# Kernel optimization log

Hardware: AMD Instinct MI355X
Metric: run time of the kernel (lower is better)

## Reference

```python
import jax, jax.numpy as jnp
import numpy as np

IN_DIM = 1024
D_QK = IN_DIM // 8  # 128


def setup_inputs() -> dict:
    key = jax.random.key(0)
    ks = jax.random.split(key, 8)
    B, S, H = 8, 2048, IN_DIM
    x = jax.random.normal(ks[0], (B, S, H), dtype=jnp.float32)
    s = 1.0 / np.sqrt(H)
    Wq = jax.random.uniform(ks[1], (H, D_QK), jnp.float32, -s, s)
    bq = jax.random.uniform(ks[2], (D_QK,), jnp.float32, -s, s)
    Wk = jax.random.uniform(ks[3], (H, D_QK), jnp.float32, -s, s)
    bk = jax.random.uniform(ks[4], (D_QK,), jnp.float32, -s, s)
    Wv = jax.random.uniform(ks[5], (H, H), jnp.float32, -s, s)
    bv = jax.random.uniform(ks[6], (H,), jnp.float32, -s, s)
    # nn.Parameter(torch.zeros(1)) in the original; use a small random value so
    # the residual-gated branch is exercised.
    gamma = jax.random.normal(ks[7], (1,), dtype=jnp.float32) * 0.1
    return {"x": x, "Wq": Wq, "bq": bq, "Wk": Wk, "bk": bk,
            "Wv": Wv, "bv": bv, "gamma": gamma}


def reference(x, Wq, bq, Wk, bk, Wv, bv, gamma):
    # x: [B, S, H]
    q = jnp.einsum('bsh,hd->bsd', x, Wq) + bq          # [B, S, D_QK]
    k = jnp.einsum('bsh,hd->bsd', x, Wk) + bk          # [B, S, D_QK]
    v = jnp.einsum('bsh,hg->bsg', x, Wv) + bv          # [B, S, H]
    energy = jnp.einsum('bsd,btd->bst', q, k)          # [B, S, S] (no 1/sqrt(d) scale, as in original)
    attention = jax.nn.softmax(energy, axis=-1)
    out = jnp.einsum('bst,bth->bsh', attention, v)     # [B, S, H]
    return gamma * out + x
```

## Files before the change

### kernel.cpp

```cpp
#include <hip/hip_runtime.h>
#include <hip/hip_bf16.h>
#include <stdint.h>


typedef __attribute__((ext_vector_type(8))) short bf16x8;
typedef __attribute__((ext_vector_type(8))) unsigned short u16x8;
typedef __attribute__((ext_vector_type(4))) float f32x4;

#define S_LEN 2048
#define NB 8
#define HDIM 1024
#define MTOT (NB * S_LEN)
#define NQKV 1280

__device__ __forceinline__ unsigned short f2b(float f) {
  union { float f; unsigned u; } v; v.f = f;
  unsigned u = v.u;
  return (unsigned short)((u + 0x7FFFu + ((u >> 16) & 1u)) >> 16);
}
__device__ __forceinline__ float b2f(unsigned short h) {
  union { unsigned u; float f; } v; v.u = ((unsigned)h) << 16; return v.f;
}

__device__ __forceinline__ void gload16(const void* g, void* l) {
  __builtin_amdgcn_global_load_lds((const __attribute__((address_space(1))) void*)g,
                                   (__attribute__((address_space(3))) void*)l,
                                   16, 0, 0);
}

__global__ void k_cast_x(const float* __restrict__ x, unsigned short* __restrict__ xb) {
  int i = blockIdx.x * blockDim.x + threadIdx.x;
  const float4* xv = (const float4*)x;
  float4 a = xv[2 * i], b = xv[2 * i + 1];
  u16x8 o;
  o[0] = f2b(a.x); o[1] = f2b(a.y); o[2] = f2b(a.z); o[3] = f2b(a.w);
  o[4] = f2b(b.x); o[5] = f2b(b.y); o[6] = f2b(b.z); o[7] = f2b(b.w);
  *(u16x8*)(xb + 8 * (size_t)i) = o;
}

__global__ void k_build_w(const float* __restrict__ Wq, const float* __restrict__ bq,
                          const float* __restrict__ Wk, const float* __restrict__ bk,
                          const float* __restrict__ Wv, const float* __restrict__ bv,
                          unsigned short* __restrict__ wt, float* __restrict__ bc) {
  int i = blockIdx.x * 256 + threadIdx.x;
  int n = i >> 10, h = i & 1023;
  float v;
  if (n < 128)      v = Wq[h * 128 + n];
  else if (n < 256) v = Wk[h * 128 + n - 128];
  else              v = Wv[h * 1024 + n - 256];
  wt[i] = f2b(v);
  if (i < NQKV) bc[i] = (i < 128) ? bq[i] : (i < 256) ? bk[i - 128] : bv[i - 256];
}

__launch_bounds__(256, 2)
__global__ void k_gemm_qkv(const unsigned short* __restrict__ A,
                           const unsigned short* __restrict__ Bt,
                           const float* __restrict__ bc,
                           unsigned short* __restrict__ C) {
  __shared__ unsigned short smem[2 * 128 * 32];
  unsigned short* As = smem;
  unsigned short* Bs = smem + 128 * 32;
  const int tid = threadIdx.x;
  const int m0 = blockIdx.x * 128, n0 = blockIdx.y * 128;
  const int l = tid & 63, wid = tid >> 6;
  const int wm = wid >> 1, wn = wid & 1;
  const int l15 = l & 15, lh = l >> 4;
  const int r0 = tid >> 2, seg = tid & 3;
  f32x4 acc[4][4] = {};
  for (int kt = 0; kt < 32; ++kt) {
#pragma unroll
    for (int p = 0; p < 2; ++p) {
      int row = p * 64 + r0;
      gload16(A  + (size_t)(m0 + row) * 1024 + kt * 32 + seg * 8, As + (size_t)(p * 256 + tid) * 8);
      gload16(Bt + (size_t)(n0 + row) * 1024 + kt * 32 + seg * 8, Bs + (size_t)(p * 256 + tid) * 8);
    }
    __syncthreads();
    bf16x8 af[4], bfr[4];
#pragma unroll
    for (int mi = 0; mi < 4; ++mi)
      af[mi] = *(const bf16x8*)&As[(wm * 64 + mi * 16 + l15) * 32 + 8 * lh];
#pragma unroll
    for (int ni = 0; ni < 4; ++ni)
      bfr[ni] = *(const bf16x8*)&Bs[(wn * 64 + ni * 16 + l15) * 32 + 8 * lh];
#pragma unroll
    for (int mi = 0; mi < 4; ++mi)
#pragma unroll
      for (int ni = 0; ni < 4; ++ni)
        acc[mi][ni] = __builtin_amdgcn_mfma_f32_16x16x32_bf16(af[mi], bfr[ni], acc[mi][ni], 0, 0, 0);
    __syncthreads();
  }
  unsigned short* sc = As + wid * 1024;
  const int erow = l >> 2, ech = l & 3;
  for (int mi = 0; mi < 4; ++mi) {
    asm volatile("s_waitcnt lgkmcnt(0)" ::: "memory");
#pragma unroll
    for (int ni = 0; ni < 4; ++ni) {
      float bias = bc[n0 + wn * 64 + ni * 16 + l15];
#pragma unroll
      for (int r = 0; r < 4; ++r) {
        int row = lh * 4 + r;
        int col = (ni * 16 + l15) ^ ((row & 7) * 8);
        sc[row * 64 + col] = f2b(acc[mi][ni][r] + bias);
      }
    }
    asm volatile("s_waitcnt lgkmcnt(0)" ::: "memory");
    int gr = m0 + wm * 64 + mi * 16 + erow;
#pragma unroll
    for (int h = 0; h < 2; ++h) {
      int ch = ech + h * 4;
      int colsw = (ch ^ (erow & 7)) * 8;
      u16x8 vv = *(const u16x8*)(sc + erow * 64 + colsw);
      *(u16x8*)(&C[(size_t)gr * NQKV + n0 + wn * 64 + ch * 8]) = vv;
    }
  }
}

__launch_bounds__(512, 2)
__global__ void k_scores(const unsigned short* __restrict__ qkv, unsigned short* __restrict__ P) {
  __shared__ unsigned short E[16 * 2048];
  const int tid = threadIdx.x;
  const int l = tid & 63, w = tid >> 6;
  const int l15 = l & 15, lh = l >> 4;
  const int b = blockIdx.y, q0 = blockIdx.x * 16;
  const size_t base = (size_t)(b * S_LEN) * NQKV;

  bf16x8 qf[4];
  const unsigned short* qrow = qkv + base + (size_t)(q0 + l15) * NQKV + 8 * lh;
#pragma unroll
  for (int d0 = 0; d0 < 4; ++d0) qf[d0] = *(const bf16x8*)(qrow + d0 * 32);

  for (int i = 0; i < 16; ++i) {
    int k0 = (w * 16 + i) * 16;
    const unsigned short* krow = qkv + base + (size_t)(k0 + l15) * NQKV + 128 + 8 * lh;
    f32x4 e = {};
#pragma unroll
    for (int d0 = 0; d0 < 4; ++d0) {
      bf16x8 kf = *(const bf16x8*)(krow + d0 * 32);
      e = __builtin_amdgcn_mfma_f32_16x16x32_bf16(qf[d0], kf, e, 0, 0, 0);
    }
#pragma unroll
    for (int r = 0; r < 4; ++r) {
      int row = lh * 4 + r;
      E[row * 2048 + ((k0 + l15) ^ (row * 8))] = f2b(e[r]);
    }
  }
  __syncthreads();

  const int r = tid >> 5, g = tid & 31;
  unsigned short* Er = &E[r * 2048];
  float mx = -3e38f;
#pragma unroll
  for (int j = 0; j < 8; ++j) {
    u16x8 v = *(const u16x8*)(Er + g * 8 + j * 256);
#pragma unroll
    for (int t = 0; t < 8; ++t) mx = fmaxf(mx, b2f(v[t]));
  }
#pragma unroll
  for (int o = 16; o; o >>= 1) mx = fmaxf(mx, __shfl_xor(mx, o));
  float sum = 0.f;
#pragma unroll
  for (int j = 0; j < 8; ++j) {
    u16x8 v = *(const u16x8*)(Er + g * 8 + j * 256);
    u16x8 ov;
#pragma unroll
    for (int t = 0; t < 8; ++t) { float e = __expf(b2f(v[t]) - mx); sum += e; ov[t] = f2b(e); }
    *(u16x8*)(Er + g * 8 + j * 256) = ov;
  }
#pragma unroll
  for (int o = 16; o; o >>= 1) sum += __shfl_xor(sum, o);
  const float inv = 1.f / sum;
  unsigned short* Pr = P + ((size_t)(b * S_LEN + q0 + r)) * S_LEN;
#pragma unroll
  for (int j = 0; j < 8; ++j) {
    int idx = g * 8 + j * 256;
    u16x8 v = *(const u16x8*)(Er + idx);
    u16x8 ov;
#pragma unroll
    for (int t = 0; t < 8; ++t) ov[t] = f2b(b2f(v[t]) * inv);
    *(u16x8*)(Pr + (idx ^ (r * 8))) = ov;
  }
}

__global__ void k_transpose_v(const unsigned short* __restrict__ qkv, unsigned short* __restrict__ vt) {
  __shared__ unsigned short t[64][66];
  const int m0 = blockIdx.x * 64, c0 = blockIdx.y * 64;
  const int tx = threadIdx.x & 63, ty = threadIdx.x >> 6;
#pragma unroll
  for (int i = 0; i < 64; i += 4)
    t[ty + i][tx] = qkv[(size_t)(m0 + ty + i) * NQKV + 256 + c0 + tx];
  __syncthreads();
#pragma unroll
  for (int i = 0; i < 64; i += 4)
    vt[(size_t)(c0 + ty + i) * MTOT + m0 + tx] = t[tx][ty + i];
}

__launch_bounds__(256, 2)
__global__ void k_gemm_pv(const unsigned short* __restrict__ P,
                          const unsigned short* __restrict__ Vt,
                          const float* __restrict__ x,
                          const float* __restrict__ gamma,
                          float* __restrict__ out) {
  __shared__ unsigned short smem[2 * 128 * 32];
  unsigned short* As = smem;
  unsigned short* Bs = smem + 128 * 32;
  const int tid = threadIdx.x;
  const int b = blockIdx.z;
  const int m0 = blockIdx.x * 128, n0 = blockIdx.y * 128;
  const int l = tid & 63, wid = tid >> 6;
  const int wm = wid >> 1, wn = wid & 1;
  const int l15 = l & 15, lh = l >> 4;
  const int r0 = tid >> 2, seg = tid & 3;
  const unsigned short* Ab = P + (size_t)b * S_LEN * S_LEN;
  f32x4 acc[4][4] = {};
  for (int kt = 0; kt < 64; ++kt) {
#pragma unroll
    for (int p = 0; p < 2; ++p) {
      int row = p * 64 + r0;
      gload16(Ab + (size_t)(m0 + row) * S_LEN + kt * 32 + seg * 8, As + (size_t)(p * 256 + tid) * 8);
      gload16(Vt + (size_t)(n0 + row) * MTOT + b * S_LEN + kt * 32 + seg * 8, Bs + (size_t)(p * 256 + tid) * 8);
    }
    __syncthreads();
    bf16x8 af[4], bfr[4];
#pragma unroll
    for (int mi = 0; mi < 4; ++mi)
      af[mi] = *(const bf16x8*)&As[(wm * 64 + mi * 16 + l15) * 32 + 8 * lh];
#pragma unroll
    for (int ni = 0; ni < 4; ++ni)
      bfr[ni] = *(const bf16x8*)&Bs[(wn * 64 + ni * 16 + l15) * 32 + 8 * lh];
#pragma unroll
    for (int mi = 0; mi < 4; ++mi)
#pragma unroll
      for (int ni = 0; ni < 4; ++ni)
        acc[mi][ni] = __builtin_amdgcn_mfma_f32_16x16x32_bf16(af[mi], bfr[ni], acc[mi][ni], 0, 0, 0);
    __syncthreads();
  }
  const float gm = gamma[0];
  float* sc = (float*)smem + wid * 1024;
  const int erow = l >> 2, ech = l & 3;
  for (int mi = 0; mi < 4; ++mi) {
    asm volatile("s_waitcnt lgkmcnt(0)" ::: "memory");
#pragma unroll
    for (int ni = 0; ni < 4; ++ni)
#pragma unroll
      for (int r = 0; r < 4; ++r) {
        int row = lh * 4 + r;
        int col = (ni * 16 + l15) ^ (row * 4);
        sc[row * 64 + col] = acc[mi][ni][r];
      }
    asm volatile("s_waitcnt lgkmcnt(0)" ::: "memory");
    int gr = b * S_LEN + m0 + wm * 64 + mi * 16 + erow;
#pragma unroll
    for (int h = 0; h < 4; ++h) {
      int ch = ech + h * 4;
      int colsw = (ch ^ erow) * 4;
      f32x4 vv = *(const f32x4*)(sc + erow * 64 + colsw);
      size_t o = (size_t)gr * HDIM + n0 + wn * 64 + ch * 4;
      float4 xv = *(const float4*)(x + o);
      float4 ov;
      ov.x = gm * vv[0] + xv.x; ov.y = gm * vv[1] + xv.y;
      ov.z = gm * vv[2] + xv.z; ov.w = gm * vv[3] + xv.w;
      *(float4*)(out + o) = ov;
    }
  }
}

extern "C" void kernel_launch(void* const* d_in, const int* in_sizes, int n_in,
                              void* d_out, int out_size, void* d_ws, size_t ws_size,
                              hipStream_t stream) {
  const float* x     = (const float*)d_in[0];
  const float* Wq    = (const float*)d_in[1];
  const float* bq    = (const float*)d_in[2];
  const float* Wk    = (const float*)d_in[3];
  const float* bk    = (const float*)d_in[4];
  const float* Wv    = (const float*)d_in[5];
  const float* bv    = (const float*)d_in[6];
  const float* gamma = (const float*)d_in[7];
  float* out = (float*)d_out;
  char* ws = (char*)d_ws;

  unsigned short* xb  = (unsigned short*)(ws);
  unsigned short* wt  = (unsigned short*)(ws + 33554432);
  float*          bc  = (float*)         (ws + 36175872);
  unsigned short* qkv = (unsigned short*)(ws + 36180992);
  unsigned short* P   = (unsigned short*)(ws + 78124032);
  unsigned short* vt  = xb;

  hipLaunchKernelGGL(k_cast_x,      dim3(8192),      dim3(256), 0, stream, x, xb);
  hipLaunchKernelGGL(k_build_w,     dim3(5120),      dim3(256), 0, stream, Wq, bq, Wk, bk, Wv, bv, wt, bc);
  hipLaunchKernelGGL(k_gemm_qkv,    dim3(128, 10),   dim3(256), 0, stream, xb, wt, bc, qkv);
  hipLaunchKernelGGL(k_scores,      dim3(128, 8),    dim3(512), 0, stream, qkv, P);
  hipLaunchKernelGGL(k_transpose_v, dim3(256, 16),   dim3(256), 0, stream, qkv, vt);
  hipLaunchKernelGGL(k_gemm_pv,     dim3(16, 8, 8),  dim3(256), 0, stream, P, vt, x, gamma, out);
}
```

Measured before the change: 366.7 us.

## Fuse scores, softmax and PV GEMM into one two-pass attention kernel

Replaces the separate score/softmax kernel, which wrote the full bf16 probability matrix to global memory, and the PV GEMM that read it back, with a single k_attn kernel. A first pass streams double-buffered K tiles and computes per-row max and sum with online rescaling. A second pass recomputes the scores, exponentiates them in LDS, and accumulates against V^T, applying gamma/L in the epilogue. This removes the large P round trip through HBM and two launches. The cost is computing QK^T twice per column half, plus a large LDS footprint that likely limits the kernel to one block per CU.

Measured after the change: 343.5 us. 6.3% less time.

```diff
diff --git a/kernel.cpp b/kernel.cpp
--- a/kernel.cpp
+++ b/kernel.cpp
@@ -26,6 +26,19 @@
   __builtin_amdgcn_global_load_lds((const __attribute__((address_space(1))) void*)g,
                                    (__attribute__((address_space(3))) void*)l,
                                    16, 0, 0);
+}
+
+__device__ __forceinline__ void bar_lgkm() {
+  asm volatile("s_waitcnt lgkmcnt(0)" ::: "memory");
+  __builtin_amdgcn_sched_barrier(0);
+  __builtin_amdgcn_s_barrier();
+  __builtin_amdgcn_sched_barrier(0);
+}
+__device__ __forceinline__ void bar_all() {
+  asm volatile("s_waitcnt vmcnt(0) lgkmcnt(0)" ::: "memory");
+  __builtin_amdgcn_sched_barrier(0);
+  __builtin_amdgcn_s_barrier();
+  __builtin_amdgcn_sched_barrier(0);
 }
 
 __global__ void k_cast_x(const float* __restrict__ x, unsigned short* __restrict__ xb) {
@@ -115,72 +128,6 @@
   }
 }
 
-__launch_bounds__(512, 2)
-__global__ void k_scores(const unsigned short* __restrict__ qkv, unsigned short* __restrict__ P) {
-  __shared__ unsigned short E[16 * 2048];
-  const int tid = threadIdx.x;
-  const int l = tid & 63, w = tid >> 6;
-  const int l15 = l & 15, lh = l >> 4;
-  const int b = blockIdx.y, q0 = blockIdx.x * 16;
-  const size_t base = (size_t)(b * S_LEN) * NQKV;
-
-  bf16x8 qf[4];
-  const unsigned short* qrow = qkv + base + (size_t)(q0 + l15) * NQKV + 8 * lh;
-#pragma unroll
-  for (int d0 = 0; d0 < 4; ++d0) qf[d0] = *(const bf16x8*)(qrow + d0 * 32);
-
-  for (int i = 0; i < 16; ++i) {
-    int k0 = (w * 16 + i) * 16;
-    const unsigned short* krow = qkv + base + (size_t)(k0 + l15) * NQKV + 128 + 8 * lh;
-    f32x4 e = {};
-#pragma unroll
-    for (int d0 = 0; d0 < 4; ++d0) {
-      bf16x8 kf = *(const bf16x8*)(krow + d0 * 32);
-      e = __builtin_amdgcn_mfma_f32_16x16x32_bf16(qf[d0], kf, e, 0, 0, 0);
-    }
-#pragma unroll
-    for (int r = 0; r < 4; ++r) {
-      int row = lh * 4 + r;
-      E[row * 2048 + ((k0 + l15) ^ (row * 8))] = f2b(e[r]);
-    }
-  }
-  __syncthreads();
-
-  const int r = tid >> 5, g = tid & 31;
-  unsigned short* Er = &E[r * 2048];
-  float mx = -3e38f;
-#pragma unroll
-  for (int j = 0; j < 8; ++j) {
-    u16x8 v = *(const u16x8*)(Er + g * 8 + j * 256);
-#pragma unroll
-    for (int t = 0; t < 8; ++t) mx = fmaxf(mx, b2f(v[t]));
-  }
-#pragma unroll
-  for (int o = 16; o; o >>= 1) mx = fmaxf(mx, __shfl_xor(mx, o));
-  float sum = 0.f;
-#pragma unroll
-  for (int j = 0; j < 8; ++j) {
-    u16x8 v = *(const u16x8*)(Er + g * 8 + j * 256);
-    u16x8 ov;
-#pragma unroll
-    for (int t = 0; t < 8; ++t) { float e = __expf(b2f(v[t]) - mx); sum += e; ov[t] = f2b(e); }
-    *(u16x8*)(Er + g * 8 + j * 256) = ov;
-  }
-#pragma unroll
-  for (int o = 16; o; o >>= 1) sum += __shfl_xor(sum, o);
-  const float inv = 1.f / sum;
-  unsigned short* Pr = P + ((size_t)(b * S_LEN + q0 + r)) * S_LEN;
-#pragma unroll
-  for (int j = 0; j < 8; ++j) {
-    int idx = g * 8 + j * 256;
-    u16x8 v = *(const u16x8*)(Er + idx);
-    u16x8 ov;
-#pragma unroll
-    for (int t = 0; t < 8; ++t) ov[t] = f2b(b2f(v[t]) * inv);
-    *(u16x8*)(Pr + (idx ^ (r * 8))) = ov;
-  }
-}
-
 __global__ void k_transpose_v(const unsigned short* __restrict__ qkv, unsigned short* __restrict__ vt) {
   __shared__ unsigned short t[64][66];
   const int m0 = blockIdx.x * 64, c0 = blockIdx.y * 64;
@@ -194,71 +141,208 @@
     vt[(size_t)(c0 + ty + i) * MTOT + m0 + tx] = t[tx][ty + i];
 }
 
-__launch_bounds__(256, 2)
-__global__ void k_gemm_pv(const unsigned short* __restrict__ P,
-                          const unsigned short* __restrict__ Vt,
-                          const float* __restrict__ x,
-                          const float* __restrict__ gamma,
-                          float* __restrict__ out) {
-  __shared__ unsigned short smem[2 * 128 * 32];
-  unsigned short* As = smem;
-  unsigned short* Bs = smem + 128 * 32;
+#define POOL_BYTES 125952
+#define QS_OFF   0
+#define PS_OFF   32768
+#define PM_OFF   32768
+#define PL_OFF   36864
+#define SM_OFF   43008
+#define SGL_OFF  43520
+#define KA0_OFF  44032
+#define KA1_OFF  76800
+#define KB0_OFF  44032
+#define KB1_OFF  52224
+#define V0_OFF   60416
+#define V1_OFF   93184
+
+__launch_bounds__(512, 2)
+__global__ void k_attn(const unsigned short* __restrict__ qkv,
+                       const unsigned short* __restrict__ vt,
+                       const float* __restrict__ x,
+                       const float* __restrict__ gamma,
+                       float* __restrict__ out) {
+  __shared__ alignas(16) char pool[POOL_BYTES];
   const int tid = threadIdx.x;
-  const int b = blockIdx.z;
-  const int m0 = blockIdx.x * 128, n0 = blockIdx.y * 128;
-  const int l = tid & 63, wid = tid >> 6;
-  const int wm = wid >> 1, wn = wid & 1;
+  const int l = tid & 63, w = tid >> 6;
   const int l15 = l & 15, lh = l >> 4;
-  const int r0 = tid >> 2, seg = tid & 3;
-  const unsigned short* Ab = P + (size_t)b * S_LEN * S_LEN;
-  f32x4 acc[4][4] = {};
+  int flat = (int)blockIdx.x + ((int)blockIdx.y << 4) + ((int)blockIdx.z << 5);
+  int nf_ = ((flat & 7) << 5) + (flat >> 3);
+  const int b = nf_ >> 5, nh = (nf_ >> 4) & 1, mt = nf_ & 15;
+  const int m0 = mt << 7;
+  const size_t rowbase = (size_t)b * S_LEN;
+
+  unsigned short* Qs = (unsigned short*)(pool + QS_OFF);
+  unsigned short* Ps = (unsigned short*)(pool + PS_OFF);
+  float* pm  = (float*)(pool + PM_OFF);
+  float* pl  = (float*)(pool + PL_OFF);
+  float* sm  = (float*)(pool + SM_OFF);
+  float* sgl = (float*)(pool + SGL_OFF);
+
+#pragma unroll
+  for (int j = 0; j < 4; ++j) {
+    int f = j * 512 + tid;
+    int qr = f >> 4, c = f & 15;
+    gload16(qkv + (rowbase + m0 + qr) * NQKV + ((c ^ (qr & 7)) * 8),
+            (void*)(pool + QS_OFF + f * 16));
+  }
+#pragma unroll
+  for (int j = 0; j < 4; ++j) {
+    int f = j * 512 + tid;
+    int kr = f >> 4, c = f & 15;
+    gload16(qkv + (rowbase + kr) * NQKV + 128 + ((c ^ (kr & 7)) * 8),
+            (void*)(pool + KA0_OFF + f * 16));
+  }
+  bar_all();
+
+  float m_p[8], l_p[8];
+#pragma unroll
+  for (int i = 0; i < 8; ++i) { m_p[i] = -3e38f; l_p[i] = 0.f; }
+
+  for (int kt = 0; kt < 16; ++kt) {
+    const char* ka = pool + ((kt & 1) ? KA1_OFF : KA0_OFF);
+    if (kt < 15) {
+      char* dst = pool + ((kt & 1) ? KA0_OFF : KA1_OFF);
+#pragma unroll
+      for (int j = 0; j < 4; ++j) {
+        int f = j * 512 + tid;
+        int kr = f >> 4, c = f & 15;
+        gload16(qkv + (rowbase + (size_t)(kt + 1) * 128 + kr) * NQKV + 128 + ((c ^ (kr & 7)) * 8),
+                (void*)(dst + f * 16));
+      }
+    }
+    bf16x8 kaf[4];
+#pragma unroll
+    for (int ds = 0; ds < 4; ++ds)
+      kaf[ds] = *(const bf16x8*)(ka + ((w * 16 + l15) * 128 + (((ds * 4 + lh) ^ (l15 & 7)) * 8)) * 2);
+#pragma unroll
+    for (int qf = 0; qf < 8; ++qf) {
+      f32x4 e = {};
+#pragma unroll
+      for (int ds = 0; ds < 4; ++ds) {
+        bf16x8 qb = *(const bf16x8*)(Qs + (qf * 16 + l15) * 128 + (((ds * 4 + lh) ^ (l15 & 7)) * 8));
+        e = __builtin_amdgcn_mfma_f32_16x16x32_bf16(kaf[ds], qb, e, 0, 0, 0);
+      }
+      float mx = fmaxf(fmaxf(e[0], e[1]), fmaxf(e[2], e[3]));
+      if (mx > m_p[qf]) { l_p[qf] *= __expf(m_p[qf] - mx); m_p[qf] = mx; }
+      l_p[qf] += __expf(e[0] - m_p[qf]) + __expf(e[1] - m_p[qf]) +
+                 __expf(e[2] - m_p[qf]) + __expf(e[3] - m_p[qf]);
+    }
+    bar_all();
+  }
+#pragma unroll
+  for (int qf = 0; qf < 8; ++qf) {
+    float m = m_p[qf], ls = l_p[qf];
+    {
+      float om = __shfl_xor(m, 16), ol = __shfl_xor(ls, 16);
+      float M = fmaxf(m, om);
+      ls = ls * __expf(m - M) + ol * __expf(om - M); m = M;
+    }
+    {
+      float om = __shfl_xor(m, 32), ol = __shfl_xor(ls, 32);
+      float M = fmaxf(m, om);
+      ls = ls * __expf(m - M) + ol * __expf(om - M); m = M;
+    }
+    if (l < 16) { pm[w * 128 + qf * 16 + l] = m; pl[w * 128 + qf * 16 + l] = ls; }
+  }
+  bar_lgkm();
+  if (tid < 128) {
+    float g0 = gamma[0];
+    float M = -3e38f, L = 0.f;
+#pragma unroll
+    for (int ww = 0; ww < 8; ++ww) {
+      float om = pm[ww * 128 + tid], ol = pl[ww * 128 + tid];
+      float M2 = fmaxf(M, om);
+      L = L * __expf(M - M2) + ol * __expf(om - M2);
+      M = M2;
+    }
+    sm[tid] = M; sgl[tid] = g0 / L;
+  }
+  bar_lgkm();
+
+  float m_r[4];
+#pragma unroll
+  for (int r = 0; r < 4; ++r) m_r[r] = sm[w * 16 + lh * 4 + r];
+
+  const size_t vtk = (size_t)b * S_LEN;
+  auto stageB = [&](int kt, int p) {
+    char* kb = pool + (p ? KB1_OFF : KB0_OFF);
+    char* vb = pool + (p ? V1_OFF : V0_OFF);
+    {
+      int key = tid >> 4, c = tid & 15;
+      gload16(qkv + (rowbase + (size_t)kt * 32 + key) * NQKV + 128 + ((c ^ (key & 7)) * 8),
+              (void*)(kb + tid * 16));
+    }
+#pragma unroll
+    for (int j = 0; j < 4; ++j) {
+      int f = j * 512 + tid;
+      int ww = f >> 8, nl = (f >> 2) & 63, kc = f & 3;
+      gload16(vt + (size_t)(nh * 512 + ww * 64 + nl) * MTOT + vtk + kt * 32 + ((kc ^ (nl & 3)) * 8),
+              (void*)(vb + f * 16));
+    }
+  };
+
+  stageB(0, 0);
+  bar_all();
+  f32x4 acc[8][4] = {};
   for (int kt = 0; kt < 64; ++kt) {
-#pragma unroll
-    for (int p = 0; p < 2; ++p) {
-      int row = p * 64 + r0;
-      gload16(Ab + (size_t)(m0 + row) * S_LEN + kt * 32 + seg * 8, As + (size_t)(p * 256 + tid) * 8);
-      gload16(Vt + (size_t)(n0 + row) * MTOT + b * S_LEN + kt * 32 + seg * 8, Bs + (size_t)(p * 256 + tid) * 8);
-    }
-    __syncthreads();
-    bf16x8 af[4], bfr[4];
-#pragma unroll
-    for (int mi = 0; mi < 4; ++mi)
-      af[mi] = *(const bf16x8*)&As[(wm * 64 + mi * 16 + l15) * 32 + 8 * lh];
-#pragma unroll
-    for (int ni = 0; ni < 4; ++ni)
-      bfr[ni] = *(const bf16x8*)&Bs[(wn * 64 + ni * 16 + l15) * 32 + 8 * lh];
-#pragma unroll
-    for (int mi = 0; mi < 4; ++mi)
-#pragma unroll
-      for (int ni = 0; ni < 4; ++ni)
-        acc[mi][ni] = __builtin_amdgcn_mfma_f32_16x16x32_bf16(af[mi], bfr[ni], acc[mi][ni], 0, 0, 0);
-    __syncthreads();
-  }
-  const float gm = gamma[0];
-  float* sc = (float*)smem + wid * 1024;
-  const int erow = l >> 2, ech = l & 3;
-  for (int mi = 0; mi < 4; ++mi) {
+    int p = kt & 1;
+    const unsigned short* kb = (const unsigned short*)(pool + (p ? KB1_OFF : KB0_OFF));
+    const unsigned short* vb = (const unsigned short*)(pool + (p ? V1_OFF : V0_OFF));
+    if (kt < 63) stageB(kt + 1, p ^ 1);
+    f32x4 s0 = {}, s1 = {};
+#pragma unroll
+    for (int ds = 0; ds < 4; ++ds) {
+      int ch = ((ds * 4 + lh) ^ (l15 & 7)) * 8;
+      bf16x8 aq = *(const bf16x8*)(Qs + (w * 16 + l15) * 128 + ch);
+      bf16x8 k0 = *(const bf16x8*)(kb + l15 * 128 + ch);
+      bf16x8 k1 = *(const bf16x8*)(kb + (16 + l15) * 128 + ch);
+      s0 = __builtin_amdgcn_mfma_f32_16x16x32_bf16(aq, k0, s0, 0, 0, 0);
+      s1 = __builtin_amdgcn_mfma_f32_16x16x32_bf16(aq, k1, s1, 0, 0, 0);
+    }
+#pragma unroll
+    for (int r = 0; r < 4; ++r) {
+      Ps[(w * 16 + lh * 4 + r) * 40 + l15]      = f2b(__expf(s0[r] - m_r[r]));
+      Ps[(w * 16 + lh * 4 + r) * 40 + 16 + l15] = f2b(__expf(s1[r] - m_r[r]));
+    }
+    bar_lgkm();
+    bf16x8 vf[4];
+#pragma unroll
+    for (int nf = 0; nf < 4; ++nf)
+      vf[nf] = *(const bf16x8*)(vb + w * 2048 + (nf * 16 + l15) * 32 + ((lh ^ (l15 & 3)) * 8));
+#pragma unroll
+    for (int mi = 0; mi < 8; ++mi) {
+      bf16x8 pa = *(const bf16x8*)(Ps + (mi * 16 + l15) * 40 + lh * 8);
+#pragma unroll
+      for (int nf = 0; nf < 4; ++nf)
+        acc[mi][nf] = __builtin_amdgcn_mfma_f32_16x16x32_bf16(pa, vf[nf], acc[mi][nf], 0, 0, 0);
+    }
+    bar_all();
+  }
+
+  float* sc = (float*)(pool + V0_OFF) + w * 1088;
+  const int row16 = l >> 2, c4 = l & 3;
+#pragma unroll
+  for (int mi = 0; mi < 8; ++mi) {
     asm volatile("s_waitcnt lgkmcnt(0)" ::: "memory");
-#pragma unroll
-    for (int ni = 0; ni < 4; ++ni)
-#pragma unroll
-      for (int r = 0; r < 4; ++r) {
-        int row = lh * 4 + r;
-        int col = (ni * 16 + l15) ^ (row * 4);
-        sc[row * 64 + col] = acc[mi][ni][r];
-      }
+    __builtin_amdgcn_sched_barrier(0);
+#pragma unroll
+    for (int nf = 0; nf < 4; ++nf)
+#pragma unroll
+      for (int r = 0; r < 4; ++r)
+        sc[(lh * 4 + r) * 68 + nf * 16 + l15] = acc[mi][nf][r];
     asm volatile("s_waitcnt lgkmcnt(0)" ::: "memory");
-    int gr = b * S_LEN + m0 + wm * 64 + mi * 16 + erow;
-#pragma unroll
-    for (int h = 0; h < 4; ++h) {
-      int ch = ech + h * 4;
-      int colsw = (ch ^ erow) * 4;
-      f32x4 vv = *(const f32x4*)(sc + erow * 64 + colsw);
-      size_t o = (size_t)gr * HDIM + n0 + wn * 64 + ch * 4;
+    __builtin_amdgcn_sched_barrier(0);
+    float scl = sgl[mi * 16 + row16];
+    size_t grow = rowbase + m0 + mi * 16 + row16;
+#pragma unroll
+    for (int g = 0; g < 4; ++g) {
+      int ch = c4 + g * 4;
+      f32x4 v = *(const f32x4*)(sc + row16 * 68 + ch * 4);
+      size_t o = grow * 1024 + (size_t)(nh * 512 + w * 64 + ch * 4);
       float4 xv = *(const float4*)(x + o);
       float4 ov;
-      ov.x = gm * vv[0] + xv.x; ov.y = gm * vv[1] + xv.y;
-      ov.z = gm * vv[2] + xv.z; ov.w = gm * vv[3] + xv.w;
+      ov.x = scl * v[0] + xv.x; ov.y = scl * v[1] + xv.y;
+      ov.z = scl * v[2] + xv.z; ov.w = scl * v[3] + xv.w;
       *(float4*)(out + o) = ov;
     }
   }
@@ -282,13 +366,11 @@
   unsigned short* wt  = (unsigned short*)(ws + 33554432);
   float*          bc  = (float*)         (ws + 36175872);
   unsigned short* qkv = (unsigned short*)(ws + 36180992);
-  unsigned short* P   = (unsigned short*)(ws + 78124032);
   unsigned short* vt  = xb;
 
   hipLaunchKernelGGL(k_cast_x,      dim3(8192),      dim3(256), 0, stream, x, xb);
   hipLaunchKernelGGL(k_build_w,     dim3(5120),      dim3(256), 0, stream, Wq, bq, Wk, bk, Wv, bv, wt, bc);
   hipLaunchKernelGGL(k_gemm_qkv,    dim3(128, 10),   dim3(256), 0, stream, xb, wt, bc, qkv);
-  hipLaunchKernelGGL(k_scores,      dim3(128, 8),    dim3(512), 0, stream, qkv, P);
   hipLaunchKernelGGL(k_transpose_v, dim3(256, 16),   dim3(256), 0, stream, qkv, vt);
-  hipLaunchKernelGGL(k_gemm_pv,     dim3(16, 8, 8),  dim3(256), 0, stream, P, vt, x, gamma, out);
-}
+  hipLaunchKernelGGL(k_attn,        dim3(16, 2, 8),  dim3(512), 0, stream, qkv, vt, x, gamma, out);
+}
```
